# Kernel tuning notes

Measured on AMD Instinct MI355X. Metric: run time of the kernel, lower is better.

Reference implementation:

```python
import jax, jax.numpy as jnp
import numpy as np
from jax import lax

NPOINT = 1024
RADIUS = 0.2
NSAMPLE = 32
BN_EPS = 1e-3  # tf_util batch_norm variance_epsilon


def setup_inputs() -> dict:
    key = jax.random.key(0)
    ks = jax.random.split(key, 16)
    B, N, Cp = 8, 4096, 64
    mlp = [64, 64, 128]
    cin = 3 + Cp  # use_xyz=True concatenates local coords
    dk, dout = 128, 128
    inp = {}
    inp["xyz"] = jax.random.uniform(ks[0], (B, N, 3), jnp.float32)
    inp["points"] = jax.random.normal(ks[1], (B, N, Cp), jnp.float32)
    dims = [cin] + mlp
    for i in range(3):
        inp[f"W{i}"] = jax.random.normal(ks[2 + i], (dims[i], dims[i + 1]), jnp.float32) / np.sqrt(dims[i]).astype(np.float32)
        inp[f"b{i}"] = jnp.zeros((dims[i + 1],), jnp.float32)
        inp[f"g{i}"] = jnp.ones((dims[i + 1],), jnp.float32)
        inp[f"be{i}"] = jnp.zeros((dims[i + 1],), jnp.float32)
    inp["Wq"] = jax.random.normal(ks[10], (3, dk), jnp.float32) * 0.1
    inp["Wk"] = jax.random.normal(ks[11], (mlp[-1], dk), jnp.float32) * 0.1
    inp["Wv"] = jax.random.normal(ks[12], (mlp[-1], dout), jnp.float32) * 0.1
    return inp


def farthest_point_sample(xyz, npoint):
    # xyz: [B, N, 3] -> idx [B, npoint] (sequential FPS, seeded at point 0)
    B, N, _ = xyz.shape

    def body(carry, _):
        dist, farthest = carry  # dist [B,N], farthest [B]
        centroid = jnp.take_along_axis(xyz, farthest[:, None, None], axis=1)  # [B,1,3]
        d = jnp.sum((xyz - centroid) ** 2, axis=-1)  # [B,N]
        dist = jnp.minimum(dist, d)
        nxt = jnp.argmax(dist, axis=-1).astype(jnp.int32)
        return (dist, nxt), farthest

    init = (jnp.full((B, N), 1e10, xyz.dtype), jnp.zeros((B,), jnp.int32))
    _, idxs = lax.scan(body, init, None, length=npoint)
    return jnp.transpose(idxs)  # [B, npoint]


def query_ball_point(radius, nsample, xyz, new_xyz):
    # first `nsample` points (in index order) within radius; pad with first hit
    N = xyz.shape[1]
    d2 = jnp.sum((new_xyz[:, :, None, :] - xyz[:, None, :, :]) ** 2, axis=-1)  # [B,S,N]
    inball = d2 < radius * radius
    ar = jnp.arange(N, dtype=jnp.int32)
    order_key = jnp.where(inball, ar, ar + N)
    idx = jnp.argsort(order_key, axis=-1)[..., :nsample].astype(jnp.int32)  # [B,S,nsample]
    valid = jnp.take_along_axis(inball, idx, axis=-1)
    idx = jnp.where(valid, idx, idx[..., :1])
    return idx


def group_point(feat, idx):
    # feat [B,N,C], idx [B,S,K] -> [B,S,K,C]
    return jax.vmap(lambda f, i: f[i])(feat, idx)


def _conv_bn_relu(x, W, b, g, be):
    y = jnp.einsum('bskc,cd->bskd', x, W) + b  # 1x1 conv == pointwise linear
    mean = jnp.mean(y, axis=(0, 1, 2))
    var = jnp.var(y, axis=(0, 1, 2))
    y = (y - mean) * g * lax.rsqrt(var + BN_EPS) + be
    return jax.nn.relu(y)


def _forward(xyz, points, Ws, bs, gs, bes, Wq, Wk, Wv):
    fps_idx = farthest_point_sample(xyz, NPOINT)                 # [B,S]
    new_xyz = jnp.take_along_axis(xyz, fps_idx[..., None], 1)    # [B,S,3]
    idx = query_ball_point(RADIUS, NSAMPLE, xyz, new_xyz)        # [B,S,K]
    grouped_xyz = group_point(xyz, idx) - new_xyz[:, :, None, :]  # local coords
    grouped_pts = group_point(points, idx)
    new_points = jnp.concatenate([grouped_xyz, grouped_pts], axis=-1)  # [B,S,K,3+C]
    for W, b, g, be in zip(Ws, bs, gs, bes):
        new_points = _conv_bn_relu(new_points, W, b, g, be)
    # attention pooling over the K neighbors, query from group center coords
    dk = Wq.shape[1]
    q = new_xyz @ Wq                                         # [B,S,dk]
    k = jnp.einsum('bskc,cd->bskd', new_points, Wk)          # [B,S,K,dk]
    v = jnp.einsum('bskc,co->bsko', new_points, Wv)          # [B,S,K,out]
    scores = jax.nn.softmax(jnp.einsum('bsd,bskd->bsk', q, k) / jnp.sqrt(jnp.float32(dk)), axis=-1)
    pooled = jnp.einsum('bsk,bsko->bso', scores, v)          # [B,S,out]
    return new_xyz, pooled, idx


def reference(xyz, points, W0, b0, g0, be0, W1, b1, g1, be1, W2, b2, g2, be2, Wq, Wk, Wv):
    return _forward(xyz, points, (W0, W1, W2), (b0, b1, b2), (g0, g1, g2), (be0, be1, be2), Wq, Wk, Wv)
```

## Files before the change

kernel.cpp:

```cpp
#include <hip/hip_runtime.h>
#include <hip/hip_bf16.h>

#define DI __device__ __forceinline__

typedef float v2f __attribute__((ext_vector_type(2)));
typedef __attribute__((ext_vector_type(8))) short bf16x8;
typedef __attribute__((ext_vector_type(4))) float f32x4;

DI float fmulr(float a, float b){ return __fmul_rn(a,b); }
DI float faddr(float a, float b){ return __fadd_rn(a,b); }
DI float fsubr(float a, float b){ return __fsub_rn(a,b); }
DI float dist2e(float x,float y,float z,float cx,float cy,float cz){
  float dx=fsubr(x,cx), dy=fsubr(y,cy), dz=fsubr(z,cz);
  return faddr(faddr(fmulr(dx,dx),fmulr(dy,dy)),fmulr(dz,dz));
}
DI unsigned short f2bf(float f){ __hip_bfloat16 h=__float2bfloat16(f); return *reinterpret_cast<unsigned short*>(&h); }

template<int C> DI float dmax_step(float x){
  int y=__builtin_amdgcn_update_dpp(0, __float_as_int(x), C, 0xF, 0xF, true);
  return fmaxf(x, __int_as_float(y));
}

__global__ __launch_bounds__(256) void fps_kernel(const float* __restrict__ xyz, float* __restrict__ out0){
  __shared__ float4 sp4[4096];
  float* spf=(float*)sp4;
  int* spi=(int*)sp4;
  int b=blockIdx.x, tid=threadIdx.x;
  const float* xb = xyz + (size_t)b*4096*3;
  for(int e=tid;e<12288;e+=256){
    int p=e/3, c=e-3*p;
    spf[4*p+c]=xb[e];
  }
  __syncthreads();
  float px[16],py[16],pz[16],dist[16];
  int p0 = tid*16;
  #pragma unroll
  for(int j=0;j<16;j++){ float4 r=sp4[p0+j]; px[j]=r.x; py[j]=r.y; pz[j]=r.z; dist[j]=1e10f; }
  int cur=0;
  float4 cc0=sp4[0];
  float cx=cc0.x, cy=cc0.y, cz=cc0.z;
  int w=tid>>6, lane=tid&63;
  int c0s=0,c1s=0,c2s=0,c3s=0;
  float* ob = out0 + (size_t)b*1024*3;
  #pragma unroll 1
  for(int t=0;t<1024;t++){
    bool mine = ((t&255)==tid);
    int hi = t>>8;
    c0s = (mine && hi==0) ? cur : c0s;
    c1s = (mine && hi==1) ? cur : c1s;
    c2s = (mine && hi==2) ? cur : c2s;
    c3s = (mine && hi==3) ? cur : c3s;
    float nd[16];
    #pragma unroll
    for(int j=0;j<16;j++){
      float d=dist2e(px[j],py[j],pz[j],cx,cy,cz);
      float m=fminf(dist[j],d); dist[j]=m; nd[j]=m;
    }
    float a0=fmaxf(nd[0],nd[1]), a1=fmaxf(nd[2],nd[3]), a2=fmaxf(nd[4],nd[5]), a3=fmaxf(nd[6],nd[7]);
    float a4=fmaxf(nd[8],nd[9]), a5=fmaxf(nd[10],nd[11]), a6=fmaxf(nd[12],nd[13]), a7=fmaxf(nd[14],nd[15]);
    float b0=fmaxf(a0,a1), b1=fmaxf(a2,a3), b2=fmaxf(a4,a5), b3=fmaxf(a6,a7);
    float bv=fmaxf(fmaxf(b0,b1),fmaxf(b2,b3));
    unsigned msk=0u;
    #pragma unroll
    for(int j=0;j<16;j++) msk |= (nd[j]==bv) ? (1u<<j) : 0u;
    int bj=__ffs(msk)-1;
    int bi=p0+bj;
    float x=bv;
    x=dmax_step<0x111>(x); x=dmax_step<0x112>(x); x=dmax_step<0x114>(x); x=dmax_step<0x118>(x);
    x=dmax_step<0x142>(x); x=dmax_step<0x143>(x);
    float wv=__int_as_float(__builtin_amdgcn_readlane(__float_as_int(x),63));
    unsigned long long em=__ballot(bv==wv);
    int L=(int)(__ffsll(em)-1);
    int wbi=__builtin_amdgcn_readlane(bi,L);
    int par=t&1;
    if(lane==0){
      spf[4*(par*8+w)+3]=wv;
      spi[4*(par*8+4+w)+3]=wbi;
    }
    __syncthreads();
    float w0=spf[4*(par*8+0)+3], w1=spf[4*(par*8+1)+3], w2=spf[4*(par*8+2)+3], w3=spf[4*(par*8+3)+3];
    int   i0=spi[4*(par*8+4)+3], i1=spi[4*(par*8+5)+3], i2=spi[4*(par*8+6)+3], i3=spi[4*(par*8+7)+3];
    float mv=fmaxf(fmaxf(w0,w1),fmaxf(w2,w3));
    int u0=(w0==mv)?i0:0x7fffffff, u1=(w1==mv)?i1:0x7fffffff;
    int u2=(w2==mv)?i2:0x7fffffff, u3=(w3==mv)?i3:0x7fffffff;
    cur=min(min(u0,u1),min(u2,u3));
    float4 cc=sp4[cur]; cx=cc.x; cy=cc.y; cz=cc.z;
  }
  { int t0=tid;     float4 c=sp4[c0s]; ob[t0*3]=c.x; ob[t0*3+1]=c.y; ob[t0*3+2]=c.z; }
  { int t1=tid+256; float4 c=sp4[c1s]; ob[t1*3]=c.x; ob[t1*3+1]=c.y; ob[t1*3+2]=c.z; }
  { int t2=tid+512; float4 c=sp4[c2s]; ob[t2*3]=c.x; ob[t2*3+1]=c.y; ob[t2*3+2]=c.z; }
  { int t3=tid+768; float4 c=sp4[c3s]; ob[t3*3]=c.x; ob[t3*3+1]=c.y; ob[t3*3+2]=c.z; }
}

__global__ __launch_bounds__(256) void ballq_kernel(const float* __restrict__ xyz, const float* __restrict__ out0,
        int* __restrict__ idxw, float* __restrict__ out2){
  __shared__ float sp[12288];
  int tid=threadIdx.x;
  int g = blockIdx.x*4 + (tid>>6);
  int lane = tid&63;
  int b = blockIdx.x>>8;
  const float* xb = xyz + (size_t)b*4096*3;
  const float4* src=(const float4*)xb; float4* dst=(float4*)sp;
  #pragma unroll
  for(int i=0;i<12;i++) dst[i*256+tid]=src[i*256+tid];
  __syncthreads();
  float cx=out0[(size_t)g*3], cy=out0[(size_t)g*3+1], cz=out0[(size_t)g*3+2];
  const float R2 = (float)(0.2*0.2);
  int cnt=0, firstp=0; bool haveFirst=false;
  for(int c=0;c<64;c++){
    int p=c*64+lane;
    float x=sp[3*p], y=sp[3*p+1], z=sp[3*p+2];
    float d2=dist2e(x,y,z,cx,cy,cz);
    bool inb = d2 < R2;
    unsigned long long mask=__ballot(inb);
    if(!haveFirst && mask){ firstp = c*64 + (__ffsll((unsigned long long)mask)-1); haveFirst=true; }
    int pos = cnt + (int)__popcll(mask & ((1ull<<lane)-1ull));
    if(inb && pos<32){ idxw[(size_t)g*32+pos]=p; out2[(size_t)g*32+pos]=(float)p; }
    cnt += (int)__popcll(mask);
    if(cnt>=32) break;
  }
  if(cnt<32){
    for(int j=cnt+lane; j<32; j+=64){ idxw[(size_t)g*32+j]=firstp; out2[(size_t)g*32+j]=(float)firstp; }
  }
}

__global__ void m_kernel(const float* __restrict__ Wq, const float* __restrict__ Wk, float* __restrict__ M){
  int c = threadIdx.x;
  float m0=0.f,m1=0.f,m2=0.f;
  for(int d=0; d<128; d++){
    float wk = Wk[c*128+d];
    m0 += Wq[d]*wk; m1 += Wq[128+d]*wk; m2 += Wq[256+d]*wk;
  }
  M[c]=m0; M[128+c]=m1; M[256+c]=m2;
}

__global__ __launch_bounds__(256) void l0_kernel(const float* __restrict__ xyz, const float* __restrict__ pts,
    const float* __restrict__ out0, const int* __restrict__ idxw,
    const float* __restrict__ W0, const float* __restrict__ b0,
    __hip_bfloat16* __restrict__ y0, float* __restrict__ P){
  __shared__ float xl[64*69];
  int tid=threadIdx.x; int base=blockIdx.x*64;
  int w=tid>>6, lane=tid&63;
  for(int i=0;i<16;i++){
    int r=w*16+i; int R=base+r;
    int g=R>>5; int b=g>>10; int p=idxw[R];
    const float* prow = pts + ((size_t)b*4096 + (size_t)p)*64;
    xl[r*69+3+lane] = prow[lane];
    if(lane<3){
      xl[r*69+lane] = fsubr(xyz[((size_t)b*4096+(size_t)p)*3+lane], out0[(size_t)g*3+lane]);
    }
  }
  __syncthreads();
  int r=tid&63;
  int cgu=__builtin_amdgcn_readfirstlane(tid>>6);
  float acc[16];
  #pragma unroll
  for(int j=0;j<16;j++) acc[j]=b0[cgu*16+j];
  for(int c=0;c<67;c++){
    float xv=xl[r*69+c];
    #pragma unroll
    for(int j=0;j<16;j++) acc[j] += xv*W0[c*64+cgu*16+j];
  }
  size_t R=(size_t)base+r;
  unsigned short tb[16];
  #pragma unroll
  for(int j=0;j<16;j++) tb[j]=f2bf(acc[j]);
  uint4* ov=(uint4*)(y0 + R*64 + cgu*16);
  ov[0]=make_uint4(tb[0]|(tb[1]<<16), tb[2]|(tb[3]<<16), tb[4]|(tb[5]<<16), tb[6]|(tb[7]<<16));
  ov[1]=make_uint4(tb[8]|(tb[9]<<16), tb[10]|(tb[11]<<16), tb[12]|(tb[13]<<16), tb[14]|(tb[15]<<16));
  #pragma unroll
  for(int j=0;j<16;j++){
    float s=acc[j], q=acc[j]*acc[j];
    #pragma unroll
    for(int m=32;m>=1;m>>=1){ s+=__shfl_xor(s,m); q+=__shfl_xor(q,m); }
    if(r==0){ P[(size_t)(cgu*16+j)*4096 + blockIdx.x]=s; P[(size_t)(128+cgu*16+j)*4096 + blockIdx.x]=q; }
  }
}

template<int CIN,int COUT>
__global__ __launch_bounds__(256) void lmid_mfma(const __hip_bfloat16* __restrict__ xin,
    const float* __restrict__ ssIn, const float* __restrict__ W, const float* __restrict__ bias,
    __hip_bfloat16* __restrict__ yout, float* __restrict__ P){
  constexpr int XS = CIN+8;
  constexpr int YS = COUT+8;
  constexpr int NT = COUT/16;
  __shared__ unsigned short xt[64*XS];
  __shared__ unsigned short wt[COUT*XS];
  __shared__ unsigned short yt[64*YS];
  __shared__ float ps[4][COUT];
  __shared__ float qs[4][COUT];
  int tid=threadIdx.x; size_t base=(size_t)blockIdx.x*64;
  int w=tid>>6, lane=tid&63;
  for(int e=tid; e<64*CIN/8; e+=256){
    int r=e/(CIN/8), c0=(e%(CIN/8))*8;
    uint4 raw = *reinterpret_cast<const uint4*>(xin + (base+(size_t)r)*CIN + c0);
    unsigned u[4]={raw.x,raw.y,raw.z,raw.w};
    unsigned short* dst=&xt[r*XS+c0];
    #pragma unroll
    for(int k2=0;k2<4;k2++){
      int c=c0+2*k2;
      float lo=__uint_as_float(u[k2]<<16);
      float hi=__uint_as_float(u[k2]&0xFFFF0000u);
      float a=lo*ssIn[c]+ssIn[128+c]; a=a>0.f?a:0.f;
      float bq=hi*ssIn[c+1]+ssIn[128+c+1]; bq=bq>0.f?bq:0.f;
      dst[2*k2]=f2bf(a); dst[2*k2+1]=f2bf(bq);
    }
  }
  for(int e=tid; e<CIN*COUT; e+=256){
    int k=e/COUT, n=e-k*COUT;
    wt[n*XS+k]=f2bf(W[e]);
  }
  __syncthreads();
  f32x4 acc[NT];
  #pragma unroll
  for(int t=0;t<NT;t++) acc[t]=(f32x4){0.f,0.f,0.f,0.f};
  int m=lane&15, kg=lane>>4;
  #pragma unroll
  for(int ks=0; ks<CIN/32; ks++){
    int k0=ks*32+kg*8;
    bf16x8 af = *(bf16x8*)&xt[(w*16+m)*XS + k0];
    #pragma unroll
    for(int t=0;t<NT;t++){
      bf16x8 bfr = *(bf16x8*)&wt[(t*16+m)*XS + k0];
      acc[t]=__builtin_amdgcn_mfma_f32_16x16x32_bf16(af,bfr,acc[t],0,0,0);
    }
  }
  #pragma unroll
  for(int t=0;t<NT;t++){
    float bv=bias[t*16+m];
    float s=0.f,q=0.f;
    #pragma unroll
    for(int rg=0;rg<4;rg++){
      float v=acc[t][rg]+bv;
      s+=v; q+=v*v;
      yt[(w*16+kg*4+rg)*YS + t*16+m]=f2bf(v);
    }
    s+=__shfl_xor(s,16); q+=__shfl_xor(q,16);
    s+=__shfl_xor(s,32); q+=__shfl_xor(q,32);
    if(kg==0){ ps[w][t*16+m]=s; qs[w][t*16+m]=q; }
  }
  __syncthreads();
  if(tid<COUT){
    float s=ps[0][tid]+ps[1][tid]+ps[2][tid]+ps[3][tid];
    float q=qs[0][tid]+qs[1][tid]+qs[2][tid]+qs[3][tid];
    P[(size_t)tid*4096+blockIdx.x]=s;
    P[(size_t)(128+tid)*4096+blockIdx.x]=q;
  }
  for(int e=tid; e<64*COUT/8; e+=256){
    int r=e/(COUT/8), c0=(e%(COUT/8))*8;
    *reinterpret_cast<uint4*>(yout + (base+(size_t)r)*COUT + c0) = *reinterpret_cast<uint4*>(&yt[r*YS+c0]);
  }
}

__global__ void fin_kernel(const float* __restrict__ P, const float* __restrict__ gg, const float* __restrict__ be,
                           float* __restrict__ ss){
  int ch=blockIdx.x; int lane=threadIdx.x;
  float s=0.f,q=0.f;
  for(int blk=lane; blk<4096; blk+=64){ s+=P[(size_t)ch*4096+blk]; q+=P[(size_t)(128+ch)*4096+blk]; }
  #pragma unroll
  for(int m=32;m>=1;m>>=1){ s+=__shfl_xor(s,m); q+=__shfl_xor(q,m); }
  if(lane==0){
    const float invNT = 1.0f/262144.0f;
    float mean=s*invNT; float var=q*invNT - mean*mean;
    float scale=gg[ch]/sqrtf(var+1e-3f);
    ss[ch]=scale; ss[128+ch]=be[ch]-mean*scale;
  }
}

__global__ __launch_bounds__(256) void sh_kernel(const __hip_bfloat16* __restrict__ y2,
    const float* __restrict__ ss2, const float* __restrict__ M, const float* __restrict__ out0,
    float* __restrict__ hbar){
  __shared__ float h[2][32*130];
  __shared__ float uLds[2][128];
  __shared__ float sLds[2][32];
  __shared__ float partLds[2][4][32];
  int tid=threadIdx.x; int grp=tid>>7, t=tid&127;
  size_t g=(size_t)blockIdx.x*2+grp;
  #pragma unroll
  for(int i=0;i<4;i++){
    int e=i*128+t;
    int row=e>>4, c0=(e&15)*8;
    uint4 raw=*reinterpret_cast<const uint4*>(y2+(g*32+(size_t)row)*128+c0);
    unsigned u[4]={raw.x,raw.y,raw.z,raw.w};
    #pragma unroll
    for(int k=0;k<4;k++){
      int c=c0+2*k;
      float lo=__uint_as_float(u[k]<<16), hi=__uint_as_float(u[k]&0xFFFF0000u);
      float a=lo*ss2[c]+ss2[128+c]; float bq=hi*ss2[c+1]+ss2[128+c+1];
      h[grp][row*130+c]  = a>0.f?a:0.f;
      h[grp][row*130+c+1]= bq>0.f?bq:0.f;
    }
  }
  float cx=out0[g*3], cy=out0[g*3+1], cz=out0[g*3+2];
  uLds[grp][t]=cx*M[t]+cy*M[128+t]+cz*M[256+t];
  __syncthreads();
  {
    int row=t&31, q=t>>5;
    float sc=0.f;
    const float* hr=&h[grp][row*130];
    const float* ur=&uLds[grp][0];
    #pragma unroll
    for(int c=0;c<32;c++) sc += hr[q*32+c]*ur[q*32+c];
    partLds[grp][q][row]=sc;
  }
  __syncthreads();
  if(t<32){
    float s=(partLds[grp][0][t]+partLds[grp][1][t])+(partLds[grp][2][t]+partLds[grp][3][t]);
    s*=0.08838834764831845f;
    float mx=s;
    #pragma unroll
    for(int m=16;m>=1;m>>=1) mx=fmaxf(mx,__shfl_xor(mx,m));
    float p=expf(s-mx);
    float sum=p;
    #pragma unroll
    for(int m=16;m>=1;m>>=1) sum+=__shfl_xor(sum,m);
    sLds[grp][t]=p/sum;
  }
  __syncthreads();
  float hb=0.f;
  for(int k=0;k<32;k++) hb+=sLds[grp][k]*h[grp][k*130+t];
  hbar[g*128+t]=hb;
}

__global__ __launch_bounds__(256) void pool_kernel(const float* __restrict__ hbar, const float* __restrict__ Wv,
    float* __restrict__ out1){
  __shared__ float xl[32*129];
  int tid=threadIdx.x; size_t g0=(size_t)blockIdx.x*32;
  for(int e=tid;e<32*128;e+=256){ int r=e>>7,ch=e&127; xl[r*129+ch]=hbar[(g0+(size_t)r)*128+ch]; }
  __syncthreads();
  int r=tid&31;
  int cgu=__builtin_amdgcn_readfirstlane(tid>>5);
  float acc[16];
  #pragma unroll
  for(int j=0;j<16;j++) acc[j]=0.f;
  for(int c=0;c<128;c++){
    float xv=xl[r*129+c];
    #pragma unroll
    for(int j=0;j<16;j++) acc[j]+=xv*Wv[c*128+cgu*16+j];
  }
  #pragma unroll
  for(int j=0;j<16;j++) out1[(g0+(size_t)r)*128+cgu*16+j]=acc[j];
}

extern "C" void kernel_launch(void* const* d_in, const int* in_sizes, int n_in,
                              void* d_out, int out_size, void* d_ws, size_t ws_size,
                              hipStream_t stream){
  (void)in_sizes; (void)n_in; (void)out_size; (void)ws_size;
  const float* xyz=(const float*)d_in[0];
  const float* pts=(const float*)d_in[1];
  const float* W0=(const float*)d_in[2];  const float* b0=(const float*)d_in[3];
  const float* g0=(const float*)d_in[4];  const float* be0=(const float*)d_in[5];
  const float* W1=(const float*)d_in[6];  const float* b1=(const float*)d_in[7];
  const float* g1=(const float*)d_in[8];  const float* be1=(const float*)d_in[9];
  const float* W2=(const float*)d_in[10]; const float* b2=(const float*)d_in[11];
  const float* g2=(const float*)d_in[12]; const float* be2=(const float*)d_in[13];
  const float* Wq=(const float*)d_in[14]; const float* Wk=(const float*)d_in[15];
  const float* Wv=(const float*)d_in[16];
  float* out0=(float*)d_out;
  float* out1=out0 + (size_t)8*1024*3;
  float* out2=out1 + (size_t)8192*128;

  char* ws=(char*)d_ws; size_t off=0;
  int* idxw=(int*)(ws+off);                    off += (size_t)8192*32*4;
  __hip_bfloat16* fa=(__hip_bfloat16*)(ws+off); off += (size_t)262144*64*2;
  __hip_bfloat16* fb=(__hip_bfloat16*)(ws+off); off += (size_t)262144*64*2;
  __hip_bfloat16* fc=(__hip_bfloat16*)(ws+off); off += (size_t)262144*128*2;
  float* P =(float*)(ws+off);                  off += (size_t)256*4096*4;
  float* ss0=(float*)(ws+off);                 off += 256*4;
  float* ss1=(float*)(ws+off);                 off += 256*4;
  float* ss2=(float*)(ws+off);                 off += 256*4;
  float* M =(float*)(ws+off);                  off += 3*128*4 + 128;
  float* hb=(float*)(ws+off);                  off += (size_t)8192*128*4;

  hipLaunchKernelGGL(fps_kernel,   dim3(8),    dim3(256),  0, stream, xyz, out0);
  hipLaunchKernelGGL(ballq_kernel, dim3(2048), dim3(256),  0, stream, xyz, out0, idxw, out2);
  hipLaunchKernelGGL(m_kernel,     dim3(1),    dim3(128),  0, stream, Wq, Wk, M);
  hipLaunchKernelGGL(l0_kernel,    dim3(4096), dim3(256),  0, stream, xyz, pts, out0, idxw, W0, b0, fa, P);
  hipLaunchKernelGGL(fin_kernel,   dim3(64),   dim3(64),   0, stream, P, g0, be0, ss0);
  hipLaunchKernelGGL((lmid_mfma<64,64>),  dim3(4096), dim3(256), 0, stream, fa, ss0, W1, b1, fb, P);
  hipLaunchKernelGGL(fin_kernel,   dim3(64),   dim3(64),   0, stream, P, g1, be1, ss1);
  hipLaunchKernelGGL((lmid_mfma<64,128>), dim3(4096), dim3(256), 0, stream, fb, ss1, W2, b2, fc, P);
  hipLaunchKernelGGL(fin_kernel,   dim3(128),  dim3(64),   0, stream, P, g2, be2, ss2);
  hipLaunchKernelGGL(sh_kernel,    dim3(4096), dim3(256),  0, stream, fc, ss2, M, out0, hb);
  hipLaunchKernelGGL(pool_kernel,  dim3(256),  dim3(256),  0, stream, hb, Wv, out1);
}
```

Baseline: 888.0 us.

## Widen FPS to 512 threads with packed 64-bit argmax and MFMA first layer

The farthest-point-sampling kernel now runs 512 threads with 8 points each, halving the serial per-thread work in each of the 1024 sequential iterations. The cross-wave argmax packs value and inverted index into a 64-bit key so an unsigned max resolves ties. The first conv layer moves from scalar FP32 FMAs to bf16 MFMA for the 64 point features, with the 3 xyz channels kept in FP32 as an initial accumulator. Per-channel BN statistics are reduced in shared memory first, and the output is written with coalesced stores. The bf16 inputs reduce precision of layer 0, and the larger block adds more wave sync overhead per FPS step.

```diff
diff --git a/kernel.cpp b/kernel.cpp
--- a/kernel.cpp
+++ b/kernel.cpp
@@ -3,7 +3,6 @@
 
 #define DI __device__ __forceinline__
 
-typedef float v2f __attribute__((ext_vector_type(2)));
 typedef __attribute__((ext_vector_type(8))) short bf16x8;
 typedef __attribute__((ext_vector_type(4))) float f32x4;
 
@@ -15,54 +14,49 @@
   return faddr(faddr(fmulr(dx,dx),fmulr(dy,dy)),fmulr(dz,dz));
 }
 DI unsigned short f2bf(float f){ __hip_bfloat16 h=__float2bfloat16(f); return *reinterpret_cast<unsigned short*>(&h); }
+DI unsigned long long umax64(unsigned long long a, unsigned long long b){ return a>b?a:b; }
 
 template<int C> DI float dmax_step(float x){
   int y=__builtin_amdgcn_update_dpp(0, __float_as_int(x), C, 0xF, 0xF, true);
   return fmaxf(x, __int_as_float(y));
 }
 
-__global__ __launch_bounds__(256) void fps_kernel(const float* __restrict__ xyz, float* __restrict__ out0){
-  __shared__ float4 sp4[4096];
-  float* spf=(float*)sp4;
-  int* spi=(int*)sp4;
+__global__ __launch_bounds__(512) void fps_kernel(const float* __restrict__ xyz, float* __restrict__ out0){
+  extern __shared__ char smem[];
+  float4* sp4=(float4*)smem;
+  float* spf=(float*)smem;
+  unsigned long long* keys=(unsigned long long*)(smem+65536);
   int b=blockIdx.x, tid=threadIdx.x;
-  const float* xb = xyz + (size_t)b*4096*3;
-  for(int e=tid;e<12288;e+=256){
-    int p=e/3, c=e-3*p;
-    spf[4*p+c]=xb[e];
-  }
-  __syncthreads();
-  float px[16],py[16],pz[16],dist[16];
-  int p0 = tid*16;
-  #pragma unroll
-  for(int j=0;j<16;j++){ float4 r=sp4[p0+j]; px[j]=r.x; py[j]=r.y; pz[j]=r.z; dist[j]=1e10f; }
+  const float* xb = xyz + (size_t)b*12288;
+  for(int e=tid;e<12288;e+=512){ int p=e/3, c=e-3*p; spf[4*p+c]=xb[e]; }
+  __syncthreads();
+  float px[8],py[8],pz[8],dist[8];
+  int p0=tid*8;
+  #pragma unroll
+  for(int j=0;j<8;j++){ float4 r=sp4[p0+j]; px[j]=r.x; py[j]=r.y; pz[j]=r.z; dist[j]=1e10f; }
   int cur=0;
   float4 cc0=sp4[0];
   float cx=cc0.x, cy=cc0.y, cz=cc0.z;
   int w=tid>>6, lane=tid&63;
-  int c0s=0,c1s=0,c2s=0,c3s=0;
+  int c0s=0,c1s=0;
   float* ob = out0 + (size_t)b*1024*3;
   #pragma unroll 1
   for(int t=0;t<1024;t++){
-    bool mine = ((t&255)==tid);
-    int hi = t>>8;
-    c0s = (mine && hi==0) ? cur : c0s;
-    c1s = (mine && hi==1) ? cur : c1s;
-    c2s = (mine && hi==2) ? cur : c2s;
-    c3s = (mine && hi==3) ? cur : c3s;
-    float nd[16];
-    #pragma unroll
-    for(int j=0;j<16;j++){
+    bool mine=((t&511)==tid);
+    int hi=t>>9;
+    c0s=(mine&&hi==0)?cur:c0s;
+    c1s=(mine&&hi==1)?cur:c1s;
+    float nd[8];
+    #pragma unroll
+    for(int j=0;j<8;j++){
       float d=dist2e(px[j],py[j],pz[j],cx,cy,cz);
       float m=fminf(dist[j],d); dist[j]=m; nd[j]=m;
     }
     float a0=fmaxf(nd[0],nd[1]), a1=fmaxf(nd[2],nd[3]), a2=fmaxf(nd[4],nd[5]), a3=fmaxf(nd[6],nd[7]);
-    float a4=fmaxf(nd[8],nd[9]), a5=fmaxf(nd[10],nd[11]), a6=fmaxf(nd[12],nd[13]), a7=fmaxf(nd[14],nd[15]);
-    float b0=fmaxf(a0,a1), b1=fmaxf(a2,a3), b2=fmaxf(a4,a5), b3=fmaxf(a6,a7);
-    float bv=fmaxf(fmaxf(b0,b1),fmaxf(b2,b3));
+    float bv=fmaxf(fmaxf(a0,a1),fmaxf(a2,a3));
     unsigned msk=0u;
     #pragma unroll
-    for(int j=0;j<16;j++) msk |= (nd[j]==bv) ? (1u<<j) : 0u;
+    for(int j=0;j<8;j++) msk |= (nd[j]==bv)?(1u<<j):0u;
     int bj=__ffs(msk)-1;
     int bi=p0+bj;
     float x=bv;
@@ -74,22 +68,20 @@
     int wbi=__builtin_amdgcn_readlane(bi,L);
     int par=t&1;
     if(lane==0){
-      spf[4*(par*8+w)+3]=wv;
-      spi[4*(par*8+4+w)+3]=wbi;
+      keys[par*8+w] = ((unsigned long long)__float_as_uint(wv)<<32)
+                    | (unsigned long long)(0xFFFFFFFFu-(unsigned)wbi);
     }
     __syncthreads();
-    float w0=spf[4*(par*8+0)+3], w1=spf[4*(par*8+1)+3], w2=spf[4*(par*8+2)+3], w3=spf[4*(par*8+3)+3];
-    int   i0=spi[4*(par*8+4)+3], i1=spi[4*(par*8+5)+3], i2=spi[4*(par*8+6)+3], i3=spi[4*(par*8+7)+3];
-    float mv=fmaxf(fmaxf(w0,w1),fmaxf(w2,w3));
-    int u0=(w0==mv)?i0:0x7fffffff, u1=(w1==mv)?i1:0x7fffffff;
-    int u2=(w2==mv)?i2:0x7fffffff, u3=(w3==mv)?i3:0x7fffffff;
-    cur=min(min(u0,u1),min(u2,u3));
+    const ulonglong2* sl2=(const ulonglong2*)(keys+par*8);
+    ulonglong2 k0=sl2[0], k1=sl2[1], k2=sl2[2], k3=sl2[3];
+    unsigned long long m0=umax64(k0.x,k0.y), m1=umax64(k1.x,k1.y);
+    unsigned long long m2=umax64(k2.x,k2.y), m3=umax64(k3.x,k3.y);
+    unsigned long long k =umax64(umax64(m0,m1),umax64(m2,m3));
+    cur=(int)(0xFFFFFFFFu-(unsigned)(k&0xFFFFFFFFull));
     float4 cc=sp4[cur]; cx=cc.x; cy=cc.y; cz=cc.z;
   }
   { int t0=tid;     float4 c=sp4[c0s]; ob[t0*3]=c.x; ob[t0*3+1]=c.y; ob[t0*3+2]=c.z; }
-  { int t1=tid+256; float4 c=sp4[c1s]; ob[t1*3]=c.x; ob[t1*3+1]=c.y; ob[t1*3+2]=c.z; }
-  { int t2=tid+512; float4 c=sp4[c2s]; ob[t2*3]=c.x; ob[t2*3+1]=c.y; ob[t2*3+2]=c.z; }
-  { int t3=tid+768; float4 c=sp4[c3s]; ob[t3*3]=c.x; ob[t3*3+1]=c.y; ob[t3*3+2]=c.z; }
+  { int t1=tid+512; float4 c=sp4[c1s]; ob[t1*3]=c.x; ob[t1*3+1]=c.y; ob[t1*3+2]=c.z; }
 }
 
 __global__ __launch_bounds__(256) void ballq_kernel(const float* __restrict__ xyz, const float* __restrict__ out0,
@@ -134,46 +126,76 @@
   M[c]=m0; M[128+c]=m1; M[256+c]=m2;
 }
 
-__global__ __launch_bounds__(256) void l0_kernel(const float* __restrict__ xyz, const float* __restrict__ pts,
+__global__ __launch_bounds__(256) void l0_mfma(const float* __restrict__ xyz, const float* __restrict__ pts,
     const float* __restrict__ out0, const int* __restrict__ idxw,
     const float* __restrict__ W0, const float* __restrict__ b0,
     __hip_bfloat16* __restrict__ y0, float* __restrict__ P){
-  __shared__ float xl[64*69];
+  __shared__ unsigned short xg[64*72];
+  __shared__ unsigned short wt[64*72];
+  __shared__ unsigned short yt[64*72];
+  __shared__ float xyzl[64][4];
+  __shared__ float w0c[3][64];
+  __shared__ float ps[4][64];
+  __shared__ float qs[4][64];
   int tid=threadIdx.x; int base=blockIdx.x*64;
   int w=tid>>6, lane=tid&63;
   for(int i=0;i<16;i++){
     int r=w*16+i; int R=base+r;
     int g=R>>5; int b=g>>10; int p=idxw[R];
-    const float* prow = pts + ((size_t)b*4096 + (size_t)p)*64;
-    xl[r*69+3+lane] = prow[lane];
-    if(lane<3){
-      xl[r*69+lane] = fsubr(xyz[((size_t)b*4096+(size_t)p)*3+lane], out0[(size_t)g*3+lane]);
-    }
-  }
-  __syncthreads();
-  int r=tid&63;
-  int cgu=__builtin_amdgcn_readfirstlane(tid>>6);
-  float acc[16];
-  #pragma unroll
-  for(int j=0;j<16;j++) acc[j]=b0[cgu*16+j];
-  for(int c=0;c<67;c++){
-    float xv=xl[r*69+c];
-    #pragma unroll
-    for(int j=0;j<16;j++) acc[j] += xv*W0[c*64+cgu*16+j];
-  }
-  size_t R=(size_t)base+r;
-  unsigned short tb[16];
-  #pragma unroll
-  for(int j=0;j<16;j++) tb[j]=f2bf(acc[j]);
-  uint4* ov=(uint4*)(y0 + R*64 + cgu*16);
-  ov[0]=make_uint4(tb[0]|(tb[1]<<16), tb[2]|(tb[3]<<16), tb[4]|(tb[5]<<16), tb[6]|(tb[7]<<16));
-  ov[1]=make_uint4(tb[8]|(tb[9]<<16), tb[10]|(tb[11]<<16), tb[12]|(tb[13]<<16), tb[14]|(tb[15]<<16));
-  #pragma unroll
-  for(int j=0;j<16;j++){
-    float s=acc[j], q=acc[j]*acc[j];
-    #pragma unroll
-    for(int m=32;m>=1;m>>=1){ s+=__shfl_xor(s,m); q+=__shfl_xor(q,m); }
-    if(r==0){ P[(size_t)(cgu*16+j)*4096 + blockIdx.x]=s; P[(size_t)(128+cgu*16+j)*4096 + blockIdx.x]=q; }
+    xg[r*72+lane] = f2bf(pts[((size_t)b*4096+(size_t)p)*64+lane]);
+    if(lane<3) xyzl[r][lane] = fsubr(xyz[((size_t)b*4096+(size_t)p)*3+lane], out0[(size_t)g*3+lane]);
+  }
+  for(int e=tid; e<4096; e+=256){
+    int k=e>>6, n=e&63;
+    wt[n*72+k]=f2bf(W0[(3+k)*64+n]);
+  }
+  if(tid<192){ int r=tid>>6, n=tid&63; w0c[r][n]=W0[r*64+n]; }
+  __syncthreads();
+  int m=lane&15, kg=lane>>4;
+  f32x4 acc[4];
+  #pragma unroll
+  for(int t=0;t<4;t++){
+    int col=t*16+m;
+    float bb=b0[col], wx=w0c[0][col], wy=w0c[1][col], wz=w0c[2][col];
+    #pragma unroll
+    for(int rg=0;rg<4;rg++){
+      int row=w*16+kg*4+rg;
+      acc[t][rg]=bb + xyzl[row][0]*wx + xyzl[row][1]*wy + xyzl[row][2]*wz;
+    }
+  }
+  #pragma unroll
+  for(int ks=0; ks<2; ks++){
+    int k0=ks*32+kg*8;
+    bf16x8 af = *(bf16x8*)&xg[(w*16+m)*72 + k0];
+    #pragma unroll
+    for(int t=0;t<4;t++){
+      bf16x8 bfr = *(bf16x8*)&wt[(t*16+m)*72 + k0];
+      acc[t]=__builtin_amdgcn_mfma_f32_16x16x32_bf16(af,bfr,acc[t],0,0,0);
+    }
+  }
+  #pragma unroll
+  for(int t=0;t<4;t++){
+    float s=0.f,q=0.f;
+    #pragma unroll
+    for(int rg=0;rg<4;rg++){
+      float v=acc[t][rg];
+      s+=v; q+=v*v;
+      yt[(w*16+kg*4+rg)*72 + t*16+m]=f2bf(v);
+    }
+    s+=__shfl_xor(s,16); q+=__shfl_xor(q,16);
+    s+=__shfl_xor(s,32); q+=__shfl_xor(q,32);
+    if(kg==0){ ps[w][t*16+m]=s; qs[w][t*16+m]=q; }
+  }
+  __syncthreads();
+  if(tid<64){
+    float s=ps[0][tid]+ps[1][tid]+ps[2][tid]+ps[3][tid];
+    float q=qs[0][tid]+qs[1][tid]+qs[2][tid]+qs[3][tid];
+    P[(size_t)tid*4096+blockIdx.x]=s;
+    P[(size_t)(128+tid)*4096+blockIdx.x]=q;
+  }
+  for(int e=tid; e<512; e+=256){
+    int r=e>>3, c0=(e&7)*8;
+    *reinterpret_cast<uint4*>(y0 + ((size_t)base+r)*64 + c0) = *reinterpret_cast<uint4*>(&yt[r*72+c0]);
   }
 }
 
@@ -372,10 +394,10 @@
   float* M =(float*)(ws+off);                  off += 3*128*4 + 128;
   float* hb=(float*)(ws+off);                  off += (size_t)8192*128*4;
 
-  hipLaunchKernelGGL(fps_kernel,   dim3(8),    dim3(256),  0, stream, xyz, out0);
+  hipLaunchKernelGGL(fps_kernel,   dim3(8),    dim3(512), 65536+128, stream, xyz, out0);
   hipLaunchKernelGGL(ballq_kernel, dim3(2048), dim3(256),  0, stream, xyz, out0, idxw, out2);
   hipLaunchKernelGGL(m_kernel,     dim3(1),    dim3(128),  0, stream, Wq, Wk, M);
-  hipLaunchKernelGGL(l0_kernel,    dim3(4096), dim3(256),  0, stream, xyz, pts, out0, idxw, W0, b0, fa, P);
+  hipLaunchKernelGGL(l0_mfma,      dim3(4096), dim3(256),  0, stream, xyz, pts, out0, idxw, W0, b0, fa, P);
   hipLaunchKernelGGL(fin_kernel,   dim3(64),   dim3(64),   0, stream, P, g0, be0, ss0);
   hipLaunchKernelGGL((lmid_mfma<64,64>),  dim3(4096), dim3(256), 0, stream, fa, ss0, W1, b1, fb, P);
   hipLaunchKernelGGL(fin_kernel,   dim3(64),   dim3(64),   0, stream, P, g1, be1, ss1);
```

Result: no change. 891.0 us (+0.3%).
